# Kernel optimization log

Hardware: AMD Instinct MI355X
Metric: run time of the kernel (lower is better)

Reference implementation:

```python
import jax, jax.numpy as jnp
import numpy as np
import math
from fractions import Fraction

L_IN, L_OUT, STEP = 4, 4, 2  # symmetric=True -> step 2 (even l only)
_SQRT2 = math.sqrt(2.0)

# ---- real Wigner 3j symbols (e3nn convention: real SH basis, unit Frobenius norm) ----

def _fact(n):
    return Fraction(math.factorial(round(n)))

def _su2_cg(j1, m1, j2, m2, j3, m3):
    if m3 != m1 + m2:
        return 0.0
    vmin = int(max(-j1 + j2 + m3, -j1 + m1, 0))
    vmax = int(min(j2 + j3 + m1, j3 - j1 + j2, j3 + m3))
    C = float(((2 * j3 + 1) * Fraction(
        _fact(j3 + j1 - j2) * _fact(j3 - j1 + j2) * _fact(j1 + j2 - j3) * _fact(j3 + m3) * _fact(j3 - m3),
        _fact(j1 + j2 + j3 + 1) * _fact(j1 - m1) * _fact(j1 + m1) * _fact(j2 - m2) * _fact(j2 + m2))) ** 0.5)
    S = Fraction(0)
    for v in range(vmin, vmax + 1):
        S += (-1) ** (v + j2 + m2) * Fraction(
            _fact(j2 + j3 + m1 - v) * _fact(j1 - m1 + v),
            _fact(v) * _fact(j3 - j1 + j2 - v) * _fact(j3 + m3 - v) * _fact(v + j1 - j2 - m3))
    return C * float(S)

def _q_real_to_complex(l):
    q = np.zeros((2 * l + 1, 2 * l + 1), dtype=np.complex128)
    for m in range(-l, 0):
        q[l + m, l + abs(m)] = 1.0 / math.sqrt(2)
        q[l + m, l - abs(m)] = -1j / math.sqrt(2)
    q[l, l] = 1.0
    for m in range(1, l + 1):
        q[l + m, l + abs(m)] = (-1) ** m / math.sqrt(2)
        q[l + m, l - abs(m)] = 1j * (-1) ** m / math.sqrt(2)
    return ((-1j) ** l) * q

def _wigner_3j(l1, l2, l3):
    C = np.zeros((2 * l1 + 1, 2 * l2 + 1, 2 * l3 + 1))
    for m1 in range(-l1, l1 + 1):
        for m2 in range(-l2, l2 + 1):
            m3 = m1 + m2
            if abs(m3) <= l3:
                C[l1 + m1, l2 + m2, l3 + m3] = _su2_cg(l1, m1, l2, m2, l3, m3)
    Q1, Q2, Q3 = _q_real_to_complex(l1), _q_real_to_complex(l2), _q_real_to_complex(l3)
    C = np.einsum('ij,kl,mn,ikn->jlm', Q1, Q2, np.conj(Q3.T), C.astype(np.complex128))
    C = np.real(C)
    nrm = np.linalg.norm(C)
    return C / nrm if nrm > 0 else C

# ---- precompute (l, l1, l2) combinations and CG tables (constants) ----
_COMBOS = []
for _l in range(0, L_OUT + 1, STEP):
    for _l1 in range(0, L_IN + 1, STEP):
        for _l2 in range(0, L_IN + 1, STEP):
            if _l2 < _l1 or abs(_l2 - _l1) > _l or _l > _l1 + _l2:
                continue
            w = _wigner_3j(_l1, _l2, _l)                  # (2l1+1, 2l2+1, 2l+1)
            cg = np.transpose(w, (2, 1, 0))               # torch .T reverses all dims
            cg_r = cg.reshape(2 * _l + 1, 2 * _l1 + 1, 2 * _l2 + 1)  # raw reshape, as in source
            cg_l = np.transpose(cg_r, (0, 2, 1))
            if _l1 != _l2:
                cg_r = _SQRT2 * cg_r
                cg_l = _SQRT2 * cg_l
            _COMBOS.append((_l, _l1, _l2,
                            jnp.asarray(cg_r, jnp.float32),
                            jnp.asarray(cg_l, jnp.float32)))


def setup_inputs() -> dict:
    key = jax.random.key(0)
    k0, k2, k4, kf = jax.random.split(key, 4)
    N, A = 16, 16
    return {
        'rh0': jax.random.normal(k0, (N, A, A, A, 1, 1), dtype=jnp.float32),
        'rh2': jax.random.normal(k2, (N, A, A, A, 5, 5), dtype=jnp.float32),
        'rh4': jax.random.normal(k4, (N, A, A, A, 9, 9), dtype=jnp.float32),
        'feats': jax.random.normal(kf, (N, 64), dtype=jnp.float32),
    }


def reference(rh0, rh2, rh4, feats):
    rh = {0: rh0, 2: rh2, 4: rh4}
    n, a, b, c = rh0.shape[:4]
    rh_n = {}
    for (l, l1, l2, cg_r, cg_l) in _COMBOS:
        # x_r: [n,a,b,c, 2l+1, (2l1+1)*(2l2+1)]
        x_r = jnp.einsum('nabcij,klj->nabckli', rh[l2], cg_r)
        x_r = x_r.reshape(n, a, b, c, 2 * l + 1, -1)
        x_l = jnp.einsum('nabcji,klj->nabckil', rh[l1], cg_l)
        x_l = x_l.reshape(n, a, b, c, 2 * l + 1, -1)
        # batched small GEMM over the fused (2l1+1)(2l2+1) axis -> [n,a,b,c,2l+1,2l+1]
        x_a = jnp.einsum('nabcki,nabcji->nabckj', x_l, x_r)
        rh_n[l] = x_a if l not in rh_n else rh_n[l] + x_a
    # rotation-invariant features
    parts = [feats]
    for l in range(0, L_OUT + 1, STEP):
        n_l = 8.0 * math.pi ** 2 / (2 * l + 1)
        fl = jnp.sum(rh_n[l] ** 2, axis=(4, 5)).reshape(n, -1)  # [n, a*b*c]
        parts.append(n_l * fl)
    feats_out = jnp.concatenate(parts, axis=1)
    return rh_n[0], rh_n[2], rh_n[4], feats_out
```

## Files before the change

### kernel.cpp

```cpp
#include <hip/hip_runtime.h>
#include <math.h>

#define DEV __device__ __forceinline__


constexpr double FC[14] = {1.,1.,2.,6.,24.,120.,720.,5040.,40320.,362880.,
                           3628800.,39916800.,479001600.,6227020800.};

constexpr double csqrt(double x) {
  if (x <= 0.0) return 0.0;
  double g = x > 1.0 ? x : 1.0;
  double p = 0.0;
  for (int i = 0; i < 64 && g != p; ++i) { p = g; g = 0.5 * (g + x / g); }
  return g;
}

constexpr int cimax(int a, int b) { return a > b ? a : b; }
constexpr int cimin(int a, int b) { return a < b ? a : b; }

constexpr double su2cg_c(int j1, int m1, int j2, int m2, int j3, int m3) {
  if (m3 != m1 + m2) return 0.0;
  int vmin = cimax(cimax(-j1 + j2 + m3, -j1 + m1), 0);
  int vmax = cimin(cimin(j2 + j3 + m1, j3 - j1 + j2), j3 + m3);
  if (vmax < vmin) return 0.0;
  double C = csqrt((2.0 * j3 + 1.0)
      * FC[j3 + j1 - j2] * FC[j3 - j1 + j2] * FC[j1 + j2 - j3]
      * FC[j3 + m3] * FC[j3 - m3]
      / (FC[j1 + j2 + j3 + 1] * FC[j1 - m1] * FC[j1 + m1]
         * FC[j2 - m2] * FC[j2 + m2]));
  double S = 0.0;
  for (int v = vmin; v <= vmax; ++v) {
    double term = FC[j2 + j3 + m1 - v] * FC[j1 - m1 + v]
        / (FC[v] * FC[j3 - j1 + j2 - v] * FC[j3 + m3 - v]
           * FC[v + j1 - j2 - m3]);
    S += ((v + j2 + m2) & 1) ? -term : term;
  }
  return C * S;
}

constexpr int nqcol(int l, int c, int* rows, double* vx, double* vy) {
  const double r2 = 0.70710678118654752440;
  double sg = (l % 4 == 2) ? -1.0 : 1.0;
  if (c == l) { rows[0] = l; vx[0] = sg; vy[0] = 0.0; return 1; }
  if (c > l) {
    int mm = c - l;
    double par = (mm & 1) ? -1.0 : 1.0;
    rows[0] = l - mm; vx[0] = sg * r2;       vy[0] = 0.0;
    rows[1] = l + mm; vx[1] = sg * par * r2; vy[1] = 0.0;
    return 2;
  }
  int mm = l - c;
  double par = (mm & 1) ? -1.0 : 1.0;
  rows[0] = l - mm; vx[0] = 0.0; vy[0] = -sg * r2;
  rows[1] = l + mm; vx[1] = 0.0; vy[1] = sg * par * r2;
  return 2;
}

constexpr int KCL [11] = {0,0,0, 2,2,2,2, 4,4,4,4};
constexpr int KCL1[11] = {0,2,4, 0,2,2,4, 0,2,2,4};
constexpr int KCL2[11] = {0,2,4, 2,2,4,4, 4,2,4,4};
constexpr int KOFF[11] = {0,1,26,107,132,257,482,887,968,1193,1598};

struct CCGT { double v[11][81]; };
constexpr CCGT make_ccg() {
  CCGT z = {};
  for (int c = 0; c < 11; ++c) {
    int l = KCL[c], l1 = KCL1[c], l2 = KCL2[c];
    int D1 = 2 * l1 + 1, D2 = 2 * l2 + 1;
    for (int a = 0; a < D1; ++a)
      for (int b = 0; b < D2; ++b) {
        int m1 = a - l1, m2 = b - l2, m3 = m1 + m2;
        z.v[c][a * D2 + b] =
            (m3 >= -l && m3 <= l) ? su2cg_c(l1, m1, l2, m2, l, m3) : 0.0;
      }
  }
  return z;
}
constexpr CCGT CCG = make_ccg();

struct CGTab { float r[2327]; float l[2327]; };
constexpr CGTab make_tables(const CCGT& cc) {
  CGTab t = {};
  for (int c = 0; c < 11; ++c) {
    int l = KCL[c], l1 = KCL1[c], l2 = KCL2[c];
    int D = 2 * l + 1, D1 = 2 * l1 + 1, D2 = 2 * l2 + 1;
    int n = D * D1 * D2, off = KOFF[c];
    double wbuf[729] = {};
    for (int e = 0; e < n; ++e) {
      int k = e % D; int ab = e / D; int b = ab % D2; int a = ab / D2;
      int r1[2] = {}, r2[2] = {}, r3[2] = {};
      double x1[2] = {}, y1[2] = {}, x2[2] = {}, y2[2] = {}, x3[2] = {}, y3[2] = {};
      int n1 = nqcol(l1, a, r1, x1, y1);
      int n2 = nqcol(l2, b, r2, x2, y2);
      int n3 = nqcol(l, k, r3, x3, y3);
      double s = 0.0;
      for (int i1 = 0; i1 < n1; ++i1)
        for (int i2 = 0; i2 < n2; ++i2) {
          double px = x1[i1] * x2[i2] - y1[i1] * y2[i2];
          double py = x1[i1] * y2[i2] + y1[i1] * x2[i2];
          int m12 = (r1[i1] - l1) + (r2[i2] - l2);
          for (int i3 = 0; i3 < n3; ++i3) {
            if (r3[i3] - l != m12) continue;
            s += (px * x3[i3] + py * y3[i3]) * cc.v[c][r1[i1] * D2 + r2[i2]];
          }
        }
      wbuf[e] = s;
    }
    double ss = 0.0;
    for (int e = 0; e < n; ++e) ss += wbuf[e] * wbuf[e];
    double inv = (l1 != l2 ? 1.41421356237309504880 : 1.0) / csqrt(ss);
    for (int o = 0; o < n; ++o) {
      int k = o / (D1 * D2), tt = o % (D1 * D2);
      int a = tt % D1, b = tt / D1;
      int x = tt / D2, y = tt % D2;
      double val = wbuf[(a * D2 + b) * D + k] * inv;
      t.r[off + o] = (float)val;
      t.l[off + k * (D1 * D2) + y * D1 + x] = (float)val;
    }
  }
  return t;
}
__constant__ CGTab G = make_tables(CCG);

__global__ void setup_copy(float* __restrict__ ws,
                           const float* __restrict__ feats,
                           float* __restrict__ out) {
  int tid = threadIdx.x;
  if (blockIdx.x == 0) {
    for (int i = tid; i < 2327; i += 256) {
      ws[i] = G.r[i];
      ws[2327 + i] = G.l[i];
    }
  } else {
    for (int i = tid; i < 1024; i += 256) {
      int n = i >> 6, j = i & 63;
      out[7012352 + n * 12352 + j] = feats[i];
    }
  }
}


template<int D, int D1, int D2>
DEV void run_combo(const float* __restrict__ cgr, const float* __restrict__ cgl,
                   const float* __restrict__ A, const float* __restrict__ B,
                   int lane, float* __restrict__ acc, int q0, int q1) {
  #pragma unroll 1
  for (int q = q0; q < q1; ++q) {
    float Brow[D2];
    #pragma unroll
    for (int j = 0; j < D2; ++j) Brow[j] = B[(q * D2 + j) * 65 + lane];
    const float* cglq = cgl + q * D1;
    #pragma unroll 1
    for (int p = 0; p < D1; ++p) {
      float Acol[D1];
      #pragma unroll
      for (int j = 0; j < D1; ++j) Acol[j] = A[(j * D1 + p) * 65 + lane];
      const float* cgrp = cgr + p * D2;
      float vl[D], vr[D];
      #pragma unroll
      for (int k = 0; k < D; ++k) {
        float s = 0.f;
        #pragma unroll
        for (int j = 0; j < D1; ++j) s = fmaf(Acol[j], cglq[k * D1 * D2 + j], s);
        vl[k] = s;
      }
      #pragma unroll
      for (int k = 0; k < D; ++k) {
        float s = 0.f;
        #pragma unroll
        for (int j = 0; j < D2; ++j) s = fmaf(Brow[j], cgrp[k * D1 * D2 + j], s);
        vr[k] = s;
      }
      #pragma unroll
      for (int k1 = 0; k1 < D; ++k1) {
        #pragma unroll
        for (int k2 = 0; k2 < D; ++k2)
          acc[k1 * D + k2] = fmaf(vl[k1], vr[k2], acc[k1 * D + k2]);
      }
    }
  }
}

__global__ __launch_bounds__(256, 2)
void quad_main(const float* __restrict__ rh0, const float* __restrict__ rh2,
               const float* __restrict__ rh4, const float* __restrict__ ws,
               float* __restrict__ out) {
  __shared__ float lds[107 * 65];
  const int tid = threadIdx.x;
  const int lane = tid & 63;
  const int wave = tid >> 6;
  const int blk = blockIdx.x;
  const int site0 = blk * 64;

  if (tid < 64) lds[tid] = rh0[site0 + tid];
  for (int f = tid; f < 1600; f += 256) {
    int s = f / 25, e = f - s * 25;
    lds[(1 + e) * 65 + s] = rh2[site0 * 25 + f];
  }
  for (int f = tid; f < 5184; f += 256) {
    int s = f / 81, e = f - s * 81;
    lds[(26 + e) * 65 + s] = rh4[site0 * 81 + f];
  }
  __syncthreads();

  const float* r0 = lds;
  const float* r2l = lds + 65;
  const float* r4l = lds + 26 * 65;
  const float* CGR = ws;
  const float* CGL = ws + 2327;

  float acc0[1] = {0.f};
  float acc2[25], acc4[81];
  #pragma unroll
  for (int i = 0; i < 25; ++i) acc2[i] = 0.f;
  #pragma unroll
  for (int i = 0; i < 81; ++i) acc4[i] = 0.f;

  if (wave == 0) {
    run_combo<9,9,9>(CGR + 1598, CGL + 1598, r4l, r4l, lane, acc4, 0, 5);
  } else if (wave == 1) {
    run_combo<5,9,9>(CGR + 482, CGL + 482, r4l, r4l, lane, acc2, 0, 9);
    run_combo<5,5,9>(CGR + 257, CGL + 257, r2l, r4l, lane, acc2, 0, 9);
  } else if (wave == 2) {
    run_combo<9,5,9>(CGR + 1193, CGL + 1193, r2l, r4l, lane, acc4, 0, 9);
    run_combo<9,5,5>(CGR + 968, CGL + 968, r2l, r2l, lane, acc4, 0, 5);
  } else {
    run_combo<9,9,9>(CGR + 1598, CGL + 1598, r4l, r4l, lane, acc4, 5, 9);
    run_combo<1,9,9>(CGR + 26, CGL + 26, r4l, r4l, lane, acc0, 0, 9);
    run_combo<9,1,9>(CGR + 887, CGL + 887, r0, r4l, lane, acc4, 0, 9);
    run_combo<5,5,5>(CGR + 132, CGL + 132, r2l, r2l, lane, acc2, 0, 5);
    run_combo<5,1,5>(CGR + 107, CGL + 107, r0, r2l, lane, acc2, 0, 5);
    run_combo<1,5,5>(CGR + 1, CGL + 1, r2l, r2l, lane, acc0, 0, 5);
    run_combo<1,1,1>(CGR + 0, CGL + 0, r0, r0, lane, acc0, 0, 1);
  }

  __syncthreads();
  if (wave == 0) {
    lds[lane] = acc0[0];
    #pragma unroll
    for (int e = 0; e < 25; ++e) lds[(1 + e) * 65 + lane] = acc2[e];
    #pragma unroll
    for (int e = 0; e < 81; ++e) lds[(26 + e) * 65 + lane] = acc4[e];
  }
  __syncthreads();
  if (wave == 1) {
    lds[lane] += acc0[0];
    #pragma unroll
    for (int e = 0; e < 25; ++e) lds[(1 + e) * 65 + lane] += acc2[e];
    #pragma unroll
    for (int e = 0; e < 81; ++e) lds[(26 + e) * 65 + lane] += acc4[e];
  }
  __syncthreads();
  if (wave == 2) {
    lds[lane] += acc0[0];
    #pragma unroll
    for (int e = 0; e < 25; ++e) lds[(1 + e) * 65 + lane] += acc2[e];
    #pragma unroll
    for (int e = 0; e < 81; ++e) lds[(26 + e) * 65 + lane] += acc4[e];
  }
  __syncthreads();
  if (wave == 3) {
    lds[lane] += acc0[0];
    #pragma unroll
    for (int e = 0; e < 25; ++e) lds[(1 + e) * 65 + lane] += acc2[e];
    #pragma unroll
    for (int e = 0; e < 81; ++e) lds[(26 + e) * 65 + lane] += acc4[e];
  }
  __syncthreads();

  if (tid < 64) out[site0 + tid] = lds[tid];
  for (int f = tid; f < 1600; f += 256) {
    int s = f / 25, e = f - s * 25;
    out[65536 + blk * 1600 + f] = lds[(1 + e) * 65 + s];
  }
  for (int f = tid; f < 5184; f += 256) {
    int s = f / 81, e = f - s * 81;
    out[1703936 + blk * 5184 + f] = lds[(26 + e) * 65 + s];
  }

  if (tid < 64) {
    int site = site0 + tid;
    int nn = site >> 12, abc = site & 4095;
    float v0 = lds[tid];
    float f0 = v0 * v0;
    float s2 = 0.f;
    #pragma unroll
    for (int e = 0; e < 25; ++e) { float v = lds[(1 + e) * 65 + tid]; s2 = fmaf(v, v, s2); }
    float s4 = 0.f;
    #pragma unroll
    for (int e = 0; e < 81; ++e) { float v = lds[(26 + e) * 65 + tid]; s4 = fmaf(v, v, s4); }
    const float PI8 = 78.95683520871486f;
    int base = 7012352 + nn * 12352 + 64;
    out[base + abc] = PI8 * f0;
    out[base + 4096 + abc] = (PI8 / 5.f) * s2;
    out[base + 8192 + abc] = (PI8 / 9.f) * s4;
  }
}

extern "C" void kernel_launch(void* const* d_in, const int* in_sizes, int n_in,
                              void* d_out, int out_size, void* d_ws, size_t ws_size,
                              hipStream_t stream) {
  const float* rh0 = (const float*)d_in[0];
  const float* rh2 = (const float*)d_in[1];
  const float* rh4 = (const float*)d_in[2];
  const float* feats = (const float*)d_in[3];
  float* out = (float*)d_out;
  float* ws = (float*)d_ws;
  setup_copy<<<2, 256, 0, stream>>>(ws, feats, out);
  quad_main<<<1024, 256, 0, stream>>>(rh0, rh2, rh4, ws, out);
}
```

Before: 205.1 us.

## Bake right CG coefficients as compile-time constants and skip zero terms

The right-side CG table is now evaluated at compile time and folded into the code as immediates. Zero coefficients are dropped from the vr contractions, and whole accumulator updates are skipped when a vr row is entirely zero. The loops are also reordered so the p loop is fully unrolled and carries the A column, while q is the runtime loop; the wave work split is rebalanced to match. This cuts global/constant loads and FMAs for the sparse Clebsch-Gordan structure, in exchange for much larger code size, longer compile times, and possible instruction-cache pressure or register spills.

```diff
diff --git a/kernel.cpp b/kernel.cpp
--- a/kernel.cpp
+++ b/kernel.cpp
@@ -1,5 +1,6 @@
 #include <hip/hip_runtime.h>
 #include <math.h>
+#include <utility>
 
 #define DEV __device__ __forceinline__
 
@@ -120,17 +121,15 @@
   }
   return t;
 }
-__constant__ CGTab G = make_tables(CCG);
+constexpr CGTab GT = make_tables(CCG);
+__constant__ CGTab G = GT;
 
 __global__ void setup_copy(float* __restrict__ ws,
                            const float* __restrict__ feats,
                            float* __restrict__ out) {
   int tid = threadIdx.x;
   if (blockIdx.x == 0) {
-    for (int i = tid; i < 2327; i += 256) {
-      ws[i] = G.r[i];
-      ws[2327 + i] = G.l[i];
-    }
+    for (int i = tid; i < 2327; i += 256) ws[i] = G.l[i];
   } else {
     for (int i = tid; i < 1024; i += 256) {
       int n = i >> 6, j = i & 63;
@@ -140,45 +139,90 @@
 }
 
 
-template<int D, int D1, int D2>
-DEV void run_combo(const float* __restrict__ cgr, const float* __restrict__ cgl,
-                   const float* __restrict__ A, const float* __restrict__ B,
-                   int lane, float* __restrict__ acc, int q0, int q1) {
+template<int OFF, int D1, int D2, int P, int K>
+constexpr bool vr_row_nz() {
+  for (int i = 0; i < D2; ++i)
+    if (GT.r[OFF + K * D1 * D2 + P * D2 + i] != 0.0f) return true;
+  return false;
+}
+
+template<int OFF, int D1, int D2, int P, int K, int I>
+DEV void vr_step(const float* __restrict__ Brow, float& s) {
+  constexpr float c = GT.r[OFF + K * D1 * D2 + P * D2 + I];
+  if constexpr (c != 0.0f) s = fmaf(Brow[I], c, s);
+}
+
+template<int OFF, int D1, int D2, int P, int K, int... Is>
+DEV float vr_k(const float* __restrict__ Brow, std::integer_sequence<int, Is...>) {
+  float s = 0.f;
+  (vr_step<OFF, D1, D2, P, K, Is>(Brow, s), ...);
+  return s;
+}
+
+template<int OFF, int D, int D1, int D2, int P, int... Ks>
+DEV void vr_all(const float* __restrict__ Brow, float* __restrict__ vr,
+                std::integer_sequence<int, Ks...>) {
+  ((vr[Ks] = vr_k<OFF, D1, D2, P, Ks>(Brow, std::make_integer_sequence<int, D2>{})), ...);
+}
+
+template<int OFF, int D, int D1, int D2, int P, int K1, int K2>
+DEV void acc_one(const float* __restrict__ vl, const float* __restrict__ vr,
+                 float* __restrict__ acc) {
+  if constexpr (vr_row_nz<OFF, D1, D2, P, K2>())
+    acc[K1 * D + K2] = fmaf(vl[K1], vr[K2], acc[K1 * D + K2]);
+}
+
+template<int OFF, int D, int D1, int D2, int P, int K1, int... K2s>
+DEV void acc_row(const float* __restrict__ vl, const float* __restrict__ vr,
+                 float* __restrict__ acc, std::integer_sequence<int, K2s...>) {
+  (acc_one<OFF, D, D1, D2, P, K1, K2s>(vl, vr, acc), ...);
+}
+
+template<int OFF, int D, int D1, int D2, int P, int... K1s>
+DEV void acc_all(const float* __restrict__ vl, const float* __restrict__ vr,
+                 float* __restrict__ acc, std::integer_sequence<int, K1s...>) {
+  (acc_row<OFF, D, D1, D2, P, K1s>(vl, vr, acc, std::make_integer_sequence<int, D>{}), ...);
+}
+
+template<int C, int D, int D1, int D2, int P>
+DEV void body(const float* __restrict__ cglws, const float* __restrict__ A,
+              const float* __restrict__ B, int lane, float* __restrict__ acc) {
+  constexpr int OFF = KOFF[C];
+  float Acol[D1];
+  #pragma unroll
+  for (int j = 0; j < D1; ++j) Acol[j] = A[(j * D1 + P) * 65 + lane];
   #pragma unroll 1
-  for (int q = q0; q < q1; ++q) {
+  for (int q = 0; q < D2; ++q) {
     float Brow[D2];
     #pragma unroll
-    for (int j = 0; j < D2; ++j) Brow[j] = B[(q * D2 + j) * 65 + lane];
-    const float* cglq = cgl + q * D1;
-    #pragma unroll 1
-    for (int p = 0; p < D1; ++p) {
-      float Acol[D1];
+    for (int i = 0; i < D2; ++i) Brow[i] = B[(q * D2 + i) * 65 + lane];
+    float vl[D];
+    #pragma unroll
+    for (int k = 0; k < D; ++k) {
+      float s = 0.f;
       #pragma unroll
-      for (int j = 0; j < D1; ++j) Acol[j] = A[(j * D1 + p) * 65 + lane];
-      const float* cgrp = cgr + p * D2;
-      float vl[D], vr[D];
-      #pragma unroll
-      for (int k = 0; k < D; ++k) {
-        float s = 0.f;
-        #pragma unroll
-        for (int j = 0; j < D1; ++j) s = fmaf(Acol[j], cglq[k * D1 * D2 + j], s);
-        vl[k] = s;
-      }
-      #pragma unroll
-      for (int k = 0; k < D; ++k) {
-        float s = 0.f;
-        #pragma unroll
-        for (int j = 0; j < D2; ++j) s = fmaf(Brow[j], cgrp[k * D1 * D2 + j], s);
-        vr[k] = s;
-      }
-      #pragma unroll
-      for (int k1 = 0; k1 < D; ++k1) {
-        #pragma unroll
-        for (int k2 = 0; k2 < D; ++k2)
-          acc[k1 * D + k2] = fmaf(vl[k1], vr[k2], acc[k1 * D + k2]);
-      }
+      for (int j = 0; j < D1; ++j)
+        s = fmaf(Acol[j], cglws[k * D1 * D2 + q * D1 + j], s);
+      vl[k] = s;
     }
-  }
+    float vr[D];
+    vr_all<OFF, D, D1, D2, P>(Brow, vr, std::make_integer_sequence<int, D>{});
+    acc_all<OFF, D, D1, D2, P>(vl, vr, acc, std::make_integer_sequence<int, D>{});
+  }
+}
+
+template<int C, int D, int D1, int D2, int P0, int... Ps>
+DEV void combo_impl(const float* __restrict__ cglws, const float* __restrict__ A,
+                    const float* __restrict__ B, int lane, float* __restrict__ acc,
+                    std::integer_sequence<int, Ps...>) {
+  (body<C, D, D1, D2, P0 + Ps>(cglws, A, B, lane, acc), ...);
+}
+
+template<int C, int D, int D1, int D2, int P0, int P1>
+DEV void combo(const float* __restrict__ ws, const float* __restrict__ A,
+               const float* __restrict__ B, int lane, float* __restrict__ acc) {
+  combo_impl<C, D, D1, D2, P0>(ws + KOFF[C], A, B, lane, acc,
+                               std::make_integer_sequence<int, P1 - P0>{});
 }
 
 __global__ __launch_bounds__(256, 2)
@@ -206,8 +250,6 @@
   const float* r0 = lds;
   const float* r2l = lds + 65;
   const float* r4l = lds + 26 * 65;
-  const float* CGR = ws;
-  const float* CGL = ws + 2327;
 
   float acc0[1] = {0.f};
   float acc2[25], acc4[81];
@@ -217,21 +259,22 @@
   for (int i = 0; i < 81; ++i) acc4[i] = 0.f;
 
   if (wave == 0) {
-    run_combo<9,9,9>(CGR + 1598, CGL + 1598, r4l, r4l, lane, acc4, 0, 5);
+    combo<10,9,9,9,0,6>(ws, r4l, r4l, lane, acc4);
   } else if (wave == 1) {
-    run_combo<5,9,9>(CGR + 482, CGL + 482, r4l, r4l, lane, acc2, 0, 9);
-    run_combo<5,5,9>(CGR + 257, CGL + 257, r2l, r4l, lane, acc2, 0, 9);
+    combo<6,5,9,9,0,9>(ws, r4l, r4l, lane, acc2);
+    combo<5,5,5,9,0,5>(ws, r2l, r4l, lane, acc2);
   } else if (wave == 2) {
-    run_combo<9,5,9>(CGR + 1193, CGL + 1193, r2l, r4l, lane, acc4, 0, 9);
-    run_combo<9,5,5>(CGR + 968, CGL + 968, r2l, r2l, lane, acc4, 0, 5);
+    combo<9,9,5,9,0,5>(ws, r2l, r4l, lane, acc4);
+    combo<8,9,5,5,0,4>(ws, r2l, r2l, lane, acc4);
   } else {
-    run_combo<9,9,9>(CGR + 1598, CGL + 1598, r4l, r4l, lane, acc4, 5, 9);
-    run_combo<1,9,9>(CGR + 26, CGL + 26, r4l, r4l, lane, acc0, 0, 9);
-    run_combo<9,1,9>(CGR + 887, CGL + 887, r0, r4l, lane, acc4, 0, 9);
-    run_combo<5,5,5>(CGR + 132, CGL + 132, r2l, r2l, lane, acc2, 0, 5);
-    run_combo<5,1,5>(CGR + 107, CGL + 107, r0, r2l, lane, acc2, 0, 5);
-    run_combo<1,5,5>(CGR + 1, CGL + 1, r2l, r2l, lane, acc0, 0, 5);
-    run_combo<1,1,1>(CGR + 0, CGL + 0, r0, r0, lane, acc0, 0, 1);
+    combo<10,9,9,9,6,9>(ws, r4l, r4l, lane, acc4);
+    combo<8,9,5,5,4,5>(ws, r2l, r2l, lane, acc4);
+    combo<7,9,1,9,0,1>(ws, r0, r4l, lane, acc4);
+    combo<4,5,5,5,0,5>(ws, r2l, r2l, lane, acc2);
+    combo<3,5,1,5,0,1>(ws, r0, r2l, lane, acc2);
+    combo<2,1,9,9,0,9>(ws, r4l, r4l, lane, acc0);
+    combo<1,1,5,5,0,5>(ws, r2l, r2l, lane, acc0);
+    combo<0,1,1,1,0,1>(ws, r0, r0, lane, acc0);
   }
 
   __syncthreads();
```

After: 171.7 us. -16.3%, faster.
